# Kernel optimization log

Measured on AMD Instinct MI355X. Metric: run time of the kernel, lower is better.

Reference implementation:

```python
import jax, jax.numpy as jnp
import numpy as np

EPS = 1e-06
NUM_HEADS = 16


def _rms_norm(x, g, eps=EPS):
    # normalize over the last (full model) dim, as WanRMSNorm(dim)
    var = jnp.mean(jnp.square(x), axis=-1, keepdims=True)
    return x * jax.lax.rsqrt(var + eps) * g


def _apply_rope(q, k, freqs):
    # q, k: [b, s, n, d]; freqs: [s, d//2] angles. Interleaved (complex) pairs
    b, s, n, d = q.shape
    cos = jnp.cos(freqs)[None, :, None, :]  # [1, s, 1, d//2]
    sin = jnp.sin(freqs)[None, :, None, :]

    def rot(t):
        tr = t.reshape(b, s, n, d // 2, 2)
        t0, t1 = tr[..., 0], tr[..., 1]
        o0 = t0 * cos - t1 * sin
        o1 = t0 * sin + t1 * cos
        return jnp.stack([o0, o1], axis=-1).reshape(b, s, n, d)

    return rot(q), rot(k)


def setup_inputs() -> dict:
    key = jax.random.key(0)
    ks = jax.random.split(key, 8)
    b, s, dim = 2, 2048, 2048
    hd = dim // NUM_HEADS
    x = jax.random.normal(ks[0], (b, s, dim), dtype=jnp.float32)
    seq_lens = jax.random.randint(ks[1], (b,), s // 2, s + 1, dtype=jnp.int32)
    grid_sizes = jax.random.randint(ks[2], (b, 3), 1, 16).astype(jnp.int64)
    freqs = jax.random.uniform(ks[3], (s, hd // 2), dtype=jnp.float32) * 6.283
    sc = 1.0 / np.sqrt(dim)
    Wq = jax.random.normal(ks[4], (dim, dim), dtype=jnp.float32) * sc
    Wk = jax.random.normal(ks[5], (dim, dim), dtype=jnp.float32) * sc
    Wv = jax.random.normal(ks[6], (dim, dim), dtype=jnp.float32) * sc
    Wo = jax.random.normal(ks[7], (dim, dim), dtype=jnp.float32) * sc
    bo = jnp.zeros((dim,), dtype=jnp.float32)
    gq = jnp.ones((dim,), dtype=jnp.float32)
    gk = jnp.ones((dim,), dtype=jnp.float32)
    return {"x": x, "seq_lens": seq_lens, "grid_sizes": grid_sizes, "freqs": freqs,
            "Wq": Wq, "Wk": Wk, "Wv": Wv, "Wo": Wo, "bo": bo, "gq": gq, "gk": gk}


def reference(x, seq_lens, grid_sizes, freqs, Wq, Wk, Wv, Wo, bo, gq, gk):
    b, s, dim = x.shape
    n = NUM_HEADS
    d = dim // n
    scale = d ** (-0.5)

    # QKV projections (Linear: x @ W.T), with RMSNorm over full dim on q/k
    q = _rms_norm(x @ Wq.T, gq).reshape(b, s, n, d)
    k = _rms_norm(x @ Wk.T, gk).reshape(b, s, n, d)
    v = (x @ Wv.T).reshape(b, s, n, d)

    q, k = _apply_rope(q, k, freqs)

    # varlen attention: keys beyond seq_lens[b] are masked out
    scores = jnp.einsum("bqnd,bknd->bnqk", q, k) * scale
    key_valid = jnp.arange(s)[None, None, None, :] < seq_lens[:, None, None, None]
    scores = jnp.where(key_valid, scores, jnp.float32(-1e9))
    probs = jax.nn.softmax(scores, axis=-1)
    attn = jnp.einsum("bnqk,bknd->bqnd", probs, v).reshape(b, s, dim)

    return attn @ Wo.T + bo
```

## Files before the change

### kernel.cpp

```cpp
#include <hip/hip_runtime.h>
#include <hip/hip_bf16.h>
#include <math.h>

#define BATCH 2
#define SEQ   2048
#define DIM   2048
#define NH    16
#define HD    128
#define NROWS (BATCH * SEQ)
#define EPS_RMS 1e-6f

typedef unsigned short ushort_t;
typedef unsigned int   uint_t;
typedef __bf16    bf16x8 __attribute__((ext_vector_type(8)));
typedef _Float16  f16x8  __attribute__((ext_vector_type(8)));
typedef float     f32x4  __attribute__((ext_vector_type(4)));

__device__ inline ushort_t f2bf(float f) {
    uint_t u = __builtin_bit_cast(uint_t, f);
    uint_t r = u + 0x7FFFu + ((u >> 16) & 1u);
    return (ushort_t)(r >> 16);
}
__device__ inline ushort_t f2h(float f) {
    return __builtin_bit_cast(ushort_t, (_Float16)f);
}

__global__ __launch_bounds__(256) void cvt_all_kernel(
    const float* __restrict__ x,  const float* __restrict__ wq,
    const float* __restrict__ wk, const float* __restrict__ wv,
    const float* __restrict__ wo,
    ushort_t* __restrict__ xh,  ushort_t* __restrict__ wqh,
    ushort_t* __restrict__ wkh, ushort_t* __restrict__ wvh,
    ushort_t* __restrict__ woh)
{
    const int blk = blockIdx.x;
    const float* src; ushort_t* dst; size_t base;
    if (blk < 4096) { src = x; dst = xh; base = (size_t)blk * 2048; }
    else {
        const int r = blk - 4096;
        const int wsel = r >> 11;
        base = (size_t)(r & 2047) * 2048;
        if      (wsel == 0) { src = wq; dst = wqh; }
        else if (wsel == 1) { src = wk; dst = wkh; }
        else if (wsel == 2) { src = wv; dst = wvh; }
        else                { src = wo; dst = woh; }
    }
    const size_t i = base + ((size_t)threadIdx.x << 3);
    float v[8];
    *(float4*)&v[0] = *(const float4*)&src[i];
    *(float4*)&v[4] = *(const float4*)&src[i + 4];
    uint_t pk[4];
#pragma unroll
    for (int j = 0; j < 4; ++j)
        pk[j] = (uint_t)f2h(v[2 * j]) | ((uint_t)f2h(v[2 * j + 1]) << 16);
    *(uint4*)&dst[i] = make_uint4(pk[0], pk[1], pk[2], pk[3]);
}

template<int MODE>
__global__ __launch_bounds__(256, 3) void gemm_f16_kernel(
    const ushort_t* __restrict__ Ah, const ushort_t* __restrict__ Bh,
    const float* __restrict__ bias,
    float* __restrict__ C, ushort_t* __restrict__ Ct,
    const int M, const int N, const int K)
{
    __shared__ __align__(16) ushort_t sA[4096], sB[4096];
    const int tid  = threadIdx.x;
    const int w    = tid >> 6;
    const int lane = tid & 63;

    const int bid   = blockIdx.x;
    const int chunk = gridDim.x >> 3;
    const int nid   = (bid & 7) * chunk + (bid >> 3);
    const int mb    = M >> 7;
    const int n_blk = nid / mb;
    const int m_blk = nid - n_blk * mb;
    const int m0 = m_blk * 128;
    const int n0 = n_blk * 128;

    const int scol = (lane & 3) << 3;
    const int wr = w >> 1, wc = w & 1;
    const int fr = lane & 15, quad = lane >> 4;

    f32x4 acc[4][4];
#pragma unroll
    for (int mi = 0; mi < 4; ++mi)
#pragma unroll
        for (int ni = 0; ni < 4; ++ni)
            acc[mi][ni] = (f32x4){0.f, 0.f, 0.f, 0.f};

    for (int k0 = 0; k0 < K; k0 += 32) {
        __syncthreads();
#pragma unroll
        for (int it = 0; it < 2; ++it) {
            const int row  = (w << 5) + (it << 4) + (lane >> 2);
            const int loff = (w << 10) + (it << 9);
            const size_t ga = (size_t)(m0 + row) * K + k0 + scol;
            const size_t gb = (size_t)(n0 + row) * K + k0 + scol;
            __builtin_amdgcn_global_load_lds(
                (const __attribute__((address_space(1))) uint_t*)(const void*)(Ah + ga),
                (__attribute__((address_space(3))) uint_t*)(void*)&sA[loff], 16, 0, 0);
            __builtin_amdgcn_global_load_lds(
                (const __attribute__((address_space(1))) uint_t*)(const void*)(Bh + gb),
                (__attribute__((address_space(3))) uint_t*)(void*)&sB[loff], 16, 0, 0);
        }
        __syncthreads();

        f16x8 bfr[4];
#pragma unroll
        for (int ni = 0; ni < 4; ++ni) {
            const int row = (wc << 6) + (ni << 4) + fr;
            bfr[ni] = *(const f16x8*)&sB[(row << 5) + (quad << 3)];
        }
#pragma unroll
        for (int mi = 0; mi < 4; ++mi) {
            const int row = (wr << 6) + (mi << 4) + fr;
            const f16x8 ah = *(const f16x8*)&sA[(row << 5) + (quad << 3)];
#pragma unroll
            for (int ni = 0; ni < 4; ++ni)
                acc[mi][ni] = __builtin_amdgcn_mfma_f32_16x16x32_f16(ah, bfr[ni], acc[mi][ni], 0, 0, 0);
        }
    }

#pragma unroll
    for (int mi = 0; mi < 4; ++mi)
#pragma unroll
        for (int ni = 0; ni < 4; ++ni) {
            const int col = n0 + (wc << 6) + (ni << 4) + fr;
            if (MODE == 0) {
                const float bv = bias ? bias[col] : 0.f;
#pragma unroll
                for (int r = 0; r < 4; ++r) {
                    const int rowg = m0 + (wr << 6) + (mi << 4) + (quad << 2) + r;
                    C[(size_t)rowg * N + col] = acc[mi][ni][r] + bv;
                }
            } else {
                const int rowg = m0 + (wr << 6) + (mi << 4) + (quad << 2);
                const int bb = rowg >> 11, tok = rowg & (SEQ - 1);
                const int hh = col >> 7, d = col & (HD - 1);
                uint2 pk;
                pk.x = (uint_t)f2bf(acc[mi][ni][0]) | ((uint_t)f2bf(acc[mi][ni][1]) << 16);
                pk.y = (uint_t)f2bf(acc[mi][ni][2]) | ((uint_t)f2bf(acc[mi][ni][3]) << 16);
                *(uint2*)&Ct[((size_t)(bb * NH + hh) * HD + d) * SEQ + tok] = pk;
            }
        }
}

__global__ __launch_bounds__(512, 2) void qkv_gemm_kernel(
    const ushort_t* __restrict__ Ah, const ushort_t* __restrict__ Bq,
    const ushort_t* __restrict__ Bk, const ushort_t* __restrict__ Bv,
    float* __restrict__ Qb, float* __restrict__ Kb, ushort_t* __restrict__ Vt)
{
    __shared__ __align__(16) ushort_t sA[16384];
    __shared__ __align__(16) ushort_t sB[32768];
    const int tid  = threadIdx.x;
    const int w    = tid >> 6;
    const int lane = tid & 63;
    const int fr   = lane & 15;
    const int quad = lane >> 4;
    const int wr   = w >> 2;
    const int wc   = w & 3;

    const int bid   = blockIdx.x;
    const int nid   = (bid & 7) * 96 + (bid >> 3);
    const int n_blk = nid >> 5;
    const int m_blk = nid & 31;
    const int wsel  = n_blk >> 3;
    const int m0    = m_blk << 7;
    const int n0    = (n_blk & 7) << 8;
    const ushort_t* __restrict__ Bh = (wsel == 0) ? Bq : (wsel == 1) ? Bk : Bv;

    const int rt  = tid >> 3;
    const int csw = ((tid & 7) ^ (rt & 7)) << 3;
    const size_t abg = (size_t)(m0 + rt) * DIM + csw;
    const size_t bbg = (size_t)(n0 + rt) * DIM + csw;
    const int lw  = w << 9;
    const int axor = (fr & 7) << 4;

#define QG(dst, src) __builtin_amdgcn_global_load_lds( \
        (const __attribute__((address_space(1))) uint_t*)(const void*)(src), \
        (__attribute__((address_space(3))) uint_t*)(void*)(dst), 16, 0, 0)
#define QSA(buf, kt, p) QG(sA + ((buf) << 13) + ((p) << 12) + lw, \
                           Ah + abg + ((size_t)(p) << 17) + ((size_t)(kt) << 6))
#define QSB(buf, kt, p) QG(sB + ((buf) << 14) + ((p) << 12) + lw, \
                           Bh + bbg + ((size_t)(p) << 17) + ((size_t)(kt) << 6))

    f32x4 acc[4][4];
#pragma unroll
    for (int mi = 0; mi < 4; ++mi)
#pragma unroll
        for (int ni = 0; ni < 4; ++ni)
            acc[mi][ni] = (f32x4){0.f, 0.f, 0.f, 0.f};

#pragma unroll
    for (int p = 0; p < 2; ++p) QSA(0, 0, p);
#pragma unroll
    for (int p = 0; p < 4; ++p) QSB(0, 0, p);
#pragma unroll
    for (int p = 0; p < 2; ++p) QSA(1, 1, p);
#pragma unroll
    for (int p = 0; p < 4; ++p) QSB(1, 1, p);
    asm volatile("s_waitcnt vmcnt(6)" ::: "memory");
    __builtin_amdgcn_sched_barrier(0);
    __builtin_amdgcn_s_barrier();
    __builtin_amdgcn_sched_barrier(0);

#define QPHASE(MB)                                                              \
        {                                                                       \
            f16x8 af[2][2];                                                     \
            _Pragma("unroll")                                                   \
            for (int m2 = 0; m2 < 2; ++m2)                                      \
                _Pragma("unroll")                                               \
                for (int ks = 0; ks < 2; ++ks)                                  \
                    af[m2][ks] = *(const f16x8*)(sAc +                          \
                        (((wr << 6) + (((MB) + m2) << 4) + fr) << 7) +          \
                        (((ks << 6) + (quad << 4)) ^ axor));                    \
            __builtin_amdgcn_s_setprio(1);                                      \
            _Pragma("unroll")                                                   \
            for (int ks = 0; ks < 2; ++ks)                                      \
                _Pragma("unroll")                                               \
                for (int m2 = 0; m2 < 2; ++m2)                                  \
                    _Pragma("unroll")                                           \
                    for (int ni = 0; ni < 4; ++ni)                              \
                        acc[(MB) + m2][ni] = __builtin_amdgcn_mfma_f32_16x16x32_f16( \
                            af[m2][ks], bfr[ni][ks], acc[(MB) + m2][ni], 0, 0, 0); \
            __builtin_amdgcn_s_setprio(0);                                      \
        }                                                                       \
        __builtin_amdgcn_sched_barrier(0);                                      \
        __builtin_amdgcn_s_barrier();                                           \
        __builtin_amdgcn_sched_barrier(0);

    for (int kt = 0; kt < 32; ++kt) {
        const int cur = kt & 1;
        const char* sAc = (const char*)sA + (cur << 14);
        const char* sBc = (const char*)sB + (cur << 15);
        const bool pf = (kt < 30);

        f16x8 bfr[4][2];
#pragma unroll
        for (int ni = 0; ni < 4; ++ni) {
            const int brow = (wc << 6) + (ni << 4) + fr;
#pragma unroll
            for (int ks = 0; ks < 2; ++ks)
                bfr[ni][ks] = *(const f16x8*)(sBc + brow * 128 +
                    (((ks << 6) + (quad << 4)) ^ axor));
        }
        QPHASE(0)
        if (pf) { QSB(cur, kt + 2, 0); QSB(cur, kt + 2, 1);
                  QSB(cur, kt + 2, 2); QSB(cur, kt + 2, 3); }
        QPHASE(2)
        if (pf) {
            QSA(cur, kt + 2, 0); QSA(cur, kt + 2, 1);
            asm volatile("s_waitcnt vmcnt(6)" ::: "memory");
        } else {
            asm volatile("s_waitcnt vmcnt(0)" ::: "memory");
        }
        __builtin_amdgcn_sched_barrier(0);
        __builtin_amdgcn_s_barrier();
        __builtin_amdgcn_sched_barrier(0);
    }
#undef QPHASE
#undef QSA
#undef QSB
#undef QG

    if (wsel < 2) {
        float* __restrict__ C = (wsel == 0) ? Qb : Kb;
#pragma unroll
        for (int mi = 0; mi < 4; ++mi)
#pragma unroll
            for (int ni = 0; ni < 4; ++ni) {
                const int col = n0 + (wc << 6) + (ni << 4) + fr;
#pragma unroll
                for (int r = 0; r < 4; ++r) {
                    const int rowg = m0 + (wr << 6) + (mi << 4) + (quad << 2) + r;
                    C[(size_t)rowg * DIM + col] = acc[mi][ni][r];
                }
            }
    } else {
#pragma unroll
        for (int mi = 0; mi < 4; ++mi)
#pragma unroll
            for (int ni = 0; ni < 4; ++ni) {
                const int col = n0 + (wc << 6) + (ni << 4) + fr;
                const int rowg = m0 + (wr << 6) + (mi << 4) + (quad << 2);
                const int bbi = rowg >> 11, tok = rowg & (SEQ - 1);
                const int hh = col >> 7, d = col & (HD - 1);
                uint2 pk;
                pk.x = (uint_t)f2bf(acc[mi][ni][0]) | ((uint_t)f2bf(acc[mi][ni][1]) << 16);
                pk.y = (uint_t)f2bf(acc[mi][ni][2]) | ((uint_t)f2bf(acc[mi][ni][3]) << 16);
                *(uint2*)&Vt[((size_t)(bbi * NH + hh) * HD + d) * SEQ + tok] = pk;
            }
    }
}

#define BM 64
#define BN 64
#define BK 16

__global__ __launch_bounds__(256) void gemm_nt_kernel(
    const float* __restrict__ A, const float* __restrict__ W,
    const float* __restrict__ bias, float* __restrict__ C,
    const int M, const int N, const int K)
{
    __shared__ float As[BK][BM + 4];
    __shared__ float Bs[BK][BN + 4];
    const int tid = threadIdx.x;
    const int tx = tid & 15;
    const int ty = tid >> 4;
    const int m0 = blockIdx.y * BM;
    const int n0 = blockIdx.x * BN;
    const int ldr = tid >> 2;
    const int ldc = (tid & 3) << 2;

    float acc[4][4] = {};

    for (int k0 = 0; k0 < K; k0 += BK) {
        __syncthreads();
        const float4 av = *(const float4*)&A[(size_t)(m0 + ldr) * K + (k0 + ldc)];
        const float4 wv = *(const float4*)&W[(size_t)(n0 + ldr) * K + (k0 + ldc)];
        As[ldc + 0][ldr] = av.x; As[ldc + 1][ldr] = av.y;
        As[ldc + 2][ldr] = av.z; As[ldc + 3][ldr] = av.w;
        Bs[ldc + 0][ldr] = wv.x; Bs[ldc + 1][ldr] = wv.y;
        Bs[ldc + 2][ldr] = wv.z; Bs[ldc + 3][ldr] = wv.w;
        __syncthreads();
#pragma unroll
        for (int k = 0; k < BK; ++k) {
            const float4 a4 = *(const float4*)&As[k][ty << 2];
            const float4 b4 = *(const float4*)&Bs[k][tx << 2];
            const float aa[4] = {a4.x, a4.y, a4.z, a4.w};
            const float bb[4] = {b4.x, b4.y, b4.z, b4.w};
#pragma unroll
            for (int i = 0; i < 4; ++i)
#pragma unroll
                for (int j = 0; j < 4; ++j)
                    acc[i][j] = fmaf(aa[i], bb[j], acc[i][j]);
        }
    }

#pragma unroll
    for (int i = 0; i < 4; ++i) {
        const int row = m0 + (ty << 2) + i;
        const int col = n0 + (tx << 2);
        float4 ov;
        ov.x = acc[i][0]; ov.y = acc[i][1]; ov.z = acc[i][2]; ov.w = acc[i][3];
        if (bias != nullptr) {
            ov.x += bias[col + 0]; ov.y += bias[col + 1];
            ov.z += bias[col + 2]; ov.w += bias[col + 3];
        }
        *(float4*)&C[(size_t)row * N + col] = ov;
    }
}

__global__ __launch_bounds__(256) void rmsnorm_rope_qk_kernel(
    const float* __restrict__ Qb, const float* __restrict__ gq,
    ushort_t* __restrict__ qbh,
    const float* __restrict__ Kb, const float* __restrict__ gk,
    ushort_t* __restrict__ kbh,
    const float* __restrict__ freqs)
{
    const int r = blockIdx.x;
    const int s = r & (SEQ - 1);
    const int tid = threadIdx.x;
    const int base = tid << 3;
    const bool isQ = (blockIdx.y == 0);
    const float* T = isQ ? Qb : Kb;
    const float* g = isQ ? gq : gk;
    ushort_t* out  = isQ ? qbh : kbh;
    const float posc = isQ ? 0.088388347648318447f : 1.0f;

    float v[8];
    *(float4*)&v[0] = *(const float4*)&T[(size_t)r * DIM + base];
    *(float4*)&v[4] = *(const float4*)&T[(size_t)r * DIM + base + 4];

    float ss = 0.f;
#pragma unroll
    for (int i = 0; i < 8; ++i) ss += v[i] * v[i];
#pragma unroll
    for (int off = 32; off > 0; off >>= 1) ss += __shfl_down(ss, off);

    __shared__ float wsum[4];
    __shared__ float inv_sh;
    if ((tid & 63) == 0) wsum[tid >> 6] = ss;
    __syncthreads();
    if (tid == 0)
        inv_sh = rsqrtf((wsum[0] + wsum[1] + wsum[2] + wsum[3]) * (1.0f / DIM) + EPS_RMS);
    __syncthreads();
    const float inv = inv_sh * posc;

    float gg[8];
    *(float4*)&gg[0] = *(const float4*)&g[base];
    *(float4*)&gg[4] = *(const float4*)&g[base + 4];
#pragma unroll
    for (int i = 0; i < 8; ++i) v[i] *= inv * gg[i];

    const int p0 = (base & (HD - 1)) >> 1;
#pragma unroll
    for (int pp = 0; pp < 4; ++pp) {
        float sn, cs;
        __sincosf(freqs[(size_t)s * (HD / 2) + p0 + pp], &sn, &cs);
        const float t0 = v[2 * pp], t1 = v[2 * pp + 1];
        v[2 * pp]     = t0 * cs - t1 * sn;
        v[2 * pp + 1] = t0 * sn + t1 * cs;
    }

    uint_t pk[4];
#pragma unroll
    for (int j = 0; j < 4; ++j)
        pk[j] = (uint_t)f2bf(v[2 * j]) | ((uint_t)f2bf(v[2 * j + 1]) << 16);
    *(uint4*)&out[(size_t)r * DIM + base] = make_uint4(pk[0], pk[1], pk[2], pk[3]);
}

__global__ __launch_bounds__(256) void rmsnorm_rope_kernel(
    float* __restrict__ T, const float* __restrict__ g,
    const float* __restrict__ freqs)
{
    const int r = blockIdx.x;
    const int s = r & (SEQ - 1);
    const int tid = threadIdx.x;
    const int base = tid << 3;

    float v[8];
    *(float4*)&v[0] = *(const float4*)&T[(size_t)r * DIM + base];
    *(float4*)&v[4] = *(const float4*)&T[(size_t)r * DIM + base + 4];

    float ss = 0.f;
#pragma unroll
    for (int i = 0; i < 8; ++i) ss += v[i] * v[i];
#pragma unroll
    for (int off = 32; off > 0; off >>= 1) ss += __shfl_down(ss, off);

    __shared__ float wsum[4];
    __shared__ float inv_sh;
    if ((tid & 63) == 0) wsum[tid >> 6] = ss;
    __syncthreads();
    if (tid == 0)
        inv_sh = rsqrtf((wsum[0] + wsum[1] + wsum[2] + wsum[3]) * (1.0f / DIM) + EPS_RMS);
    __syncthreads();
    const float inv = inv_sh;

    float gg[8];
    *(float4*)&gg[0] = *(const float4*)&g[base];
    *(float4*)&gg[4] = *(const float4*)&g[base + 4];
#pragma unroll
    for (int i = 0; i < 8; ++i) v[i] *= inv * gg[i];

    const int p0 = (base & (HD - 1)) >> 1;
#pragma unroll
    for (int pp = 0; pp < 4; ++pp) {
        float sn, cs;
        __sincosf(freqs[(size_t)s * (HD / 2) + p0 + pp], &sn, &cs);
        const float t0 = v[2 * pp], t1 = v[2 * pp + 1];
        v[2 * pp]     = t0 * cs - t1 * sn;
        v[2 * pp + 1] = t0 * sn + t1 * cs;
    }

    *(float4*)&T[(size_t)r * DIM + base]     = *(float4*)&v[0];
    *(float4*)&T[(size_t)r * DIM + base + 4] = *(float4*)&v[4];
}

#define AQ 128
#define AK 64
#define KSTR 136
#define VSTR 72
#define RESCALE_THR 8.0f

__global__ __launch_bounds__(256, 3) void attn_mfma_kernel(
    const ushort_t* __restrict__ QH, const ushort_t* __restrict__ KH,
    const ushort_t* __restrict__ VtG, const int* __restrict__ seq_lens,
    ushort_t* __restrict__ Oh)
{
    __shared__ __align__(16) ushort_t sK[AK * KSTR];
    __shared__ __align__(16) ushort_t sVt[HD * VSTR];
    __shared__ __align__(16) ushort_t sP[AQ * VSTR];

    const int tid  = threadIdx.x;
    const int w    = tid >> 6;
    const int lane = tid & 63;
    const int fr   = lane & 15;
    const int quad = lane >> 4;

    const int bid = blockIdx.x;
    const int sw  = (bid & 7) * 64 + (bid >> 3);
    const int q0  = (sw & 15) * AQ;
    const int hb  = sw >> 4;
    const int h   = hb & 15;
    const int b   = hb >> 4;
    const int len = seq_lens[b];

    bf16x8 qfrag[2][4];
#pragma unroll
    for (int qt = 0; qt < 2; ++qt)
#pragma unroll
        for (int h4 = 0; h4 < 4; ++h4) {
            const size_t qrow = (size_t)(b * SEQ + q0 + (w << 5) + (qt << 4) + fr);
            qfrag[qt][h4] = *(const bf16x8*)&QH[qrow * DIM + h * HD + (h4 << 5) + (quad << 3)];
        }

    f32x4 Oacc[2][8];
#pragma unroll
    for (int qt = 0; qt < 2; ++qt)
#pragma unroll
        for (int dt = 0; dt < 8; ++dt)
            Oacc[qt][dt] = (f32x4){0.f, 0.f, 0.f, 0.f};
    float mrow[2] = {-1.0e30f, -1.0e30f};
    float lrow[2] = {0.f, 0.f};

    const int kr  = tid >> 4;
    const int kc8 = (tid & 15) << 3;
    const int vd  = tid >> 3;
    const int vc8 = (tid & 7) << 3;
    const size_t kbase = (size_t)(b * SEQ) * DIM + h * HD + kc8;
    const size_t vbase = ((size_t)(b * NH + h) * HD) * SEQ + vc8;

    const int ntiles = (len + AK - 1) / AK;
    for (int t = 0; t < ntiles; ++t) {
        const int k0 = t * AK;
        const bool masked = (k0 + AK > len);
        __syncthreads();
        {
            uint4 kv[4], vv[4];
#pragma unroll
            for (int j = 0; j < 4; ++j)
                kv[j] = *(const uint4*)&KH[kbase + (size_t)(k0 + kr + (j << 4)) * DIM];
#pragma unroll
            for (int j = 0; j < 4; ++j)
                vv[j] = *(const uint4*)&VtG[vbase + (size_t)(vd + (j << 5)) * SEQ + k0];
#pragma unroll
            for (int j = 0; j < 4; ++j)
                *(uint4*)&sK[(kr + (j << 4)) * KSTR + kc8] = kv[j];
#pragma unroll
            for (int j = 0; j < 4; ++j)
                *(uint4*)&sVt[(vd + (j << 5)) * VSTR + vc8] = vv[j];
        }
        __syncthreads();

        f32x4 S[4][2];
        __builtin_amdgcn_s_setprio(1);
#pragma unroll
        for (int kt = 0; kt < 4; ++kt) {
            bf16x8 kf[4];
#pragma unroll
            for (int h4 = 0; h4 < 4; ++h4)
                kf[h4] = *(const bf16x8*)&sK[((kt << 4) + fr) * KSTR + (h4 << 5) + (quad << 3)];
#pragma unroll
            for (int qt = 0; qt < 2; ++qt) {
                f32x4 a = (f32x4){0.f, 0.f, 0.f, 0.f};
#pragma unroll
                for (int h4 = 0; h4 < 4; ++h4)
                    a = __builtin_amdgcn_mfma_f32_16x16x32_bf16(kf[h4], qfrag[qt][h4], a, 0, 0, 0);
                S[kt][qt] = a;
            }
        }
        __builtin_amdgcn_s_setprio(0);

#pragma unroll
        for (int qt = 0; qt < 2; ++qt) {
            float tm = -1.0e30f;
            if (masked) {
#pragma unroll
                for (int kt = 0; kt < 4; ++kt)
#pragma unroll
                    for (int r = 0; r < 4; ++r) {
                        const int key = k0 + (kt << 4) + (quad << 2) + r;
                        float s = (key < len) ? S[kt][qt][r] : -1.0e30f;
                        S[kt][qt][r] = s;
                        tm = fmaxf(tm, s);
                    }
            } else {
#pragma unroll
                for (int kt = 0; kt < 4; ++kt)
#pragma unroll
                    for (int r = 0; r < 4; ++r)
                        tm = fmaxf(tm, S[kt][qt][r]);
            }
            tm = fmaxf(tm, __shfl_xor(tm, 16));
            tm = fmaxf(tm, __shfl_xor(tm, 32));

            float mnew;
            if (__all(tm - mrow[qt] <= RESCALE_THR)) {
                mnew = mrow[qt];
            } else {
                mnew = fmaxf(mrow[qt], tm);
                const float alpha = __expf(mrow[qt] - mnew);
                mrow[qt] = mnew;
                lrow[qt] *= alpha;
#pragma unroll
                for (int r = 0; r < 4; ++r) {
                    const float ar = __shfl(alpha, (quad << 2) + r);
#pragma unroll
                    for (int dt = 0; dt < 8; ++dt)
                        Oacc[qt][dt][r] *= ar;
                }
            }

            float rsum = 0.f;
#pragma unroll
            for (int kt = 0; kt < 4; ++kt) {
                float p[4];
#pragma unroll
                for (int r = 0; r < 4; ++r) {
                    p[r] = __expf(S[kt][qt][r] - mnew);
                    rsum += p[r];
                }
                uint2 pk;
                pk.x = (uint_t)f2bf(p[0]) | ((uint_t)f2bf(p[1]) << 16);
                pk.y = (uint_t)f2bf(p[2]) | ((uint_t)f2bf(p[3]) << 16);
                *(uint2*)&sP[((w << 5) + (qt << 4) + fr) * VSTR + (kt << 4) + (quad << 2)] = pk;
            }
            rsum += __shfl_xor(rsum, 16);
            rsum += __shfl_xor(rsum, 32);
            lrow[qt] += rsum;
        }

        __builtin_amdgcn_s_setprio(1);
#pragma unroll
        for (int ks = 0; ks < 2; ++ks) {
            bf16x8 pf[2];
#pragma unroll
            for (int qt = 0; qt < 2; ++qt)
                pf[qt] = *(const bf16x8*)&sP[((w << 5) + (qt << 4) + fr) * VSTR + (ks << 5) + (quad << 3)];
#pragma unroll
            for (int dt = 0; dt < 8; ++dt) {
                const bf16x8 vf = *(const bf16x8*)&sVt[((dt << 4) + fr) * VSTR + (ks << 5) + (quad << 3)];
#pragma unroll
                for (int qt = 0; qt < 2; ++qt)
                    Oacc[qt][dt] = __builtin_amdgcn_mfma_f32_16x16x32_bf16(pf[qt], vf, Oacc[qt][dt], 0, 0, 0);
            }
        }
        __builtin_amdgcn_s_setprio(0);
    }

#pragma unroll
    for (int qt = 0; qt < 2; ++qt) {
        float linv[4];
#pragma unroll
        for (int r = 0; r < 4; ++r)
            linv[r] = 1.0f / __shfl(lrow[qt], (quad << 2) + r);
#pragma unroll
        for (int dt = 0; dt < 8; ++dt)
#pragma unroll
            for (int r = 0; r < 4; ++r) {
                const int qrow = q0 + (w << 5) + (qt << 4) + (quad << 2) + r;
                Oh[(size_t)(b * SEQ + qrow) * DIM + h * HD + (dt << 4) + fr] =
                    f2h(Oacc[qt][dt][r] * linv[r]);
            }
    }
}

#define BQ  64
#define BKT 64

__global__ __launch_bounds__(256) void attn_kernel(
    const float* __restrict__ Q, const float* __restrict__ K,
    const float* __restrict__ V, const int* __restrict__ seq_lens,
    float* __restrict__ O)
{
    const int qt = blockIdx.x;
    const int h  = blockIdx.y;
    const int b  = blockIdx.z;
    const int len = seq_lens[b];
    const int q0 = qt * BQ;
    const float scale = 0.088388347648318447f;

    __shared__ float Qst[HD][BQ + 4];
    __shared__ float Kst[HD][BKT + 4];
    __shared__ float Vs[BKT][HD + 4];
    __shared__ float Sc[BQ][BKT + 1];
    __shared__ float mrow[BQ], lrow[BQ], alpha_s[BQ];

    const int tid = threadIdx.x;
    const int si0 = (tid >> 4) << 2;
    const int sj0 = (tid & 15) << 2;
    const int pi0 = (tid >> 4) << 2;
    const int pc0 = (tid & 15) << 3;

    for (int i = tid; i < BQ * HD / 4; i += 256) {
        const int e = i << 2;
        const int row = e >> 7;
        const int c0 = e & (HD - 1);
        const float4 qv = *(const float4*)&Q[(size_t)(b * SEQ + q0 + row) * DIM + h * HD + c0];
        Qst[c0 + 0][row] = qv.x; Qst[c0 + 1][row] = qv.y;
        Qst[c0 + 2][row] = qv.z; Qst[c0 + 3][row] = qv.w;
    }
    if (tid < BQ) { mrow[tid] = -3.0e38f; lrow[tid] = 0.f; }

    float o[4][8] = {};
    __syncthreads();

    const int ntiles = (len + BKT - 1) / BKT;
    for (int t = 0; t < ntiles; ++t) {
        const int k0 = t * BKT;
        __syncthreads();
        for (int i = tid; i < BKT * HD / 4; i += 256) {
            const int e = i << 2;
            const int row = e >> 7;
            const int c0 = e & (HD - 1);
            const int kg = k0 + row;
            float4 kv = make_float4(0.f, 0.f, 0.f, 0.f);
            float4 vv = make_float4(0.f, 0.f, 0.f, 0.f);
            if (kg < len) {
                kv = *(const float4*)&K[(size_t)(b * SEQ + kg) * DIM + h * HD + c0];
                vv = *(const float4*)&V[(size_t)(b * SEQ + kg) * DIM + h * HD + c0];
            }
            Kst[c0 + 0][row] = kv.x; Kst[c0 + 1][row] = kv.y;
            Kst[c0 + 2][row] = kv.z; Kst[c0 + 3][row] = kv.w;
            *(float4*)&Vs[row][c0] = vv;
        }
        __syncthreads();

        float acc[4][4] = {};
#pragma unroll 8
        for (int kk = 0; kk < HD; ++kk) {
            const float4 q4 = *(const float4*)&Qst[kk][si0];
            const float4 k4 = *(const float4*)&Kst[kk][sj0];
            const float qa[4] = {q4.x, q4.y, q4.z, q4.w};
            const float ka[4] = {k4.x, k4.y, k4.z, k4.w};
#pragma unroll
            for (int i = 0; i < 4; ++i)
#pragma unroll
                for (int j = 0; j < 4; ++j)
                    acc[i][j] = fmaf(qa[i], ka[j], acc[i][j]);
        }
#pragma unroll
        for (int i = 0; i < 4; ++i)
#pragma unroll
            for (int j = 0; j < 4; ++j) {
                const int jg = k0 + sj0 + j;
                Sc[si0 + i][sj0 + j] = (jg < len) ? acc[i][j] * scale : -1.0e9f;
            }
        __syncthreads();

        if (tid < BQ) {
            const int i = tid;
            const float m_old = mrow[i];
            float mx = m_old;
            for (int j = 0; j < BKT; ++j) mx = fmaxf(mx, Sc[i][j]);
            const float al = __expf(m_old - mx);
            float sum = 0.f;
            for (int j = 0; j < BKT; ++j) {
                const float p = __expf(Sc[i][j] - mx);
                Sc[i][j] = p;
                sum += p;
            }
            mrow[i] = mx;
            lrow[i] = lrow[i] * al + sum;
            alpha_s[i] = al;
        }
        __syncthreads();

#pragma unroll
        for (int i = 0; i < 4; ++i) {
            const float al = alpha_s[pi0 + i];
#pragma unroll
            for (int c = 0; c < 8; ++c) o[i][c] *= al;
        }
        for (int j = 0; j < BKT; ++j) {
            float p[4];
#pragma unroll
            for (int i = 0; i < 4; ++i) p[i] = Sc[pi0 + i][j];
            const float4 v0 = *(const float4*)&Vs[j][pc0];
            const float4 v1 = *(const float4*)&Vs[j][pc0 + 4];
            const float va[8] = {v0.x, v0.y, v0.z, v0.w, v1.x, v1.y, v1.z, v1.w};
#pragma unroll
            for (int i = 0; i < 4; ++i)
#pragma unroll
                for (int c = 0; c < 8; ++c)
                    o[i][c] = fmaf(p[i], va[c], o[i][c]);
        }
    }

#pragma unroll
    for (int i = 0; i < 4; ++i) {
        const float invl = 1.0f / lrow[pi0 + i];
        float4 w0, w1;
        w0.x = o[i][0] * invl; w0.y = o[i][1] * invl;
        w0.z = o[i][2] * invl; w0.w = o[i][3] * invl;
        w1.x = o[i][4] * invl; w1.y = o[i][5] * invl;
        w1.z = o[i][6] * invl; w1.w = o[i][7] * invl;
        float* op = &O[(size_t)(b * SEQ + q0 + pi0 + i) * DIM + h * HD + pc0];
        *(float4*)&op[0] = w0;
        *(float4*)&op[4] = w1;
    }
}

extern "C" void kernel_launch(void* const* d_in, const int* in_sizes, int n_in,
                              void* d_out, int out_size, void* d_ws, size_t ws_size,
                              hipStream_t stream)
{
    const float* x        = (const float*)d_in[0];
    const int*   seq_lens = (const int*)d_in[1];
    const float* freqs    = (const float*)d_in[3];
    const float* Wq       = (const float*)d_in[4];
    const float* Wk       = (const float*)d_in[5];
    const float* Wv       = (const float*)d_in[6];
    const float* Wo       = (const float*)d_in[7];
    const float* bo       = (const float*)d_in[8];
    const float* gq       = (const float*)d_in[9];
    const float* gk       = (const float*)d_in[10];
    float* out = (float*)d_out;

    const size_t mat = (size_t)NROWS * DIM;
    const size_t wsz = (size_t)DIM * DIM;

    float*    Qb   = (float*)d_ws;
    float*    Kb   = Qb + mat;
    ushort_t* xh   = (ushort_t*)(Kb + mat);
    ushort_t* wqh  = xh + mat;
    ushort_t* wkh  = wqh + wsz;
    ushort_t* wvh  = wkh + wsz;
    ushort_t* woh  = wvh + wsz;
    ushort_t* qbh  = woh + wsz;
    ushort_t* kbh  = qbh + mat;
    ushort_t* vtg  = kbh + mat;
    ushort_t* abh  = vtg + mat;

    const size_t need = 2 * mat * sizeof(float)
                      + (mat + 4 * wsz + 4 * mat) * sizeof(ushort_t);

    if (ws_size >= need) {
        cvt_all_kernel<<<12288, 256, 0, stream>>>(
            x, Wq, Wk, Wv, Wo, xh, wqh, wkh, wvh, woh);

        qkv_gemm_kernel<<<768, 512, 0, stream>>>(xh, wqh, wkh, wvh, Qb, Kb, vtg);

        rmsnorm_rope_qk_kernel<<<dim3(NROWS, 2), 256, 0, stream>>>(
            Qb, gq, qbh, Kb, gk, kbh, freqs);

        attn_mfma_kernel<<<512, 256, 0, stream>>>(qbh, kbh, vtg, seq_lens, abh);

        gemm_f16_kernel<0><<<512, 256, 0, stream>>>(abh, woh, bo, out, nullptr, NROWS, DIM, DIM);
    } else {
        float* Vb = Kb + mat;
        float* Ab = Vb + mat;
        const dim3 gemm_grid(DIM / BN, NROWS / BM);
        gemm_nt_kernel<<<gemm_grid, 256, 0, stream>>>(x, Wq, nullptr, Qb, NROWS, DIM, DIM);
        gemm_nt_kernel<<<gemm_grid, 256, 0, stream>>>(x, Wk, nullptr, Kb, NROWS, DIM, DIM);
        gemm_nt_kernel<<<gemm_grid, 256, 0, stream>>>(x, Wv, nullptr, Vb, NROWS, DIM, DIM);
        rmsnorm_rope_kernel<<<NROWS, 256, 0, stream>>>(Qb, gq, freqs);
        rmsnorm_rope_kernel<<<NROWS, 256, 0, stream>>>(Kb, gk, freqs);
        attn_kernel<<<dim3(SEQ / BQ, NH, BATCH), 256, 0, stream>>>(Qb, Kb, Vb, seq_lens, Ab);
        gemm_nt_kernel<<<gemm_grid, 256, 0, stream>>>(Ab, Wo, bo, out, NROWS, DIM, DIM);
    }
}
```

Measured before the change: 452.4 us.

## Triple-buffer QKV GEMM LDS tiles and issue prefetch at iteration start

The QKV projection GEMM moves from a two-slot LDS ring, where next-tile loads were interleaved between MFMA phases, to a three-slot ring. All loads for tile kt+2 are issued at the top of each iteration into a free slot. The intra-iteration barriers and sched_barriers go away, leaving one wait and one barrier per k-step, which is meant to reduce synchronisation stalls and widen load/compute overlap. LDS use grows from 96KB to 144KB per block, which can cut the two-blocks-per-CU occupancy implied by the launch bounds. The waitcnt of 6 on the last prefetched iteration now also covers fewer outstanding loads, so correctness depends on the count still matching.

```diff
diff --git a/kernel.cpp b/kernel.cpp
--- a/kernel.cpp
+++ b/kernel.cpp
@@ -150,8 +150,8 @@
     const ushort_t* __restrict__ Bk, const ushort_t* __restrict__ Bv,
     float* __restrict__ Qb, float* __restrict__ Kb, ushort_t* __restrict__ Vt)
 {
-    __shared__ __align__(16) ushort_t sA[16384];
-    __shared__ __align__(16) ushort_t sB[32768];
+    __shared__ __align__(16) ushort_t sA[24576];
+    __shared__ __align__(16) ushort_t sB[49152];
     const int tid  = threadIdx.x;
     const int w    = tid >> 6;
     const int lane = tid & 63;
@@ -179,10 +179,12 @@
 #define QG(dst, src) __builtin_amdgcn_global_load_lds( \
         (const __attribute__((address_space(1))) uint_t*)(const void*)(src), \
         (__attribute__((address_space(3))) uint_t*)(void*)(dst), 16, 0, 0)
-#define QSA(buf, kt, p) QG(sA + ((buf) << 13) + ((p) << 12) + lw, \
+#define QSA(buf, kt, p) QG(sA + (buf) * 8192 + ((p) << 12) + lw, \
                            Ah + abg + ((size_t)(p) << 17) + ((size_t)(kt) << 6))
-#define QSB(buf, kt, p) QG(sB + ((buf) << 14) + ((p) << 12) + lw, \
+#define QSB(buf, kt, p) QG(sB + (buf) * 16384 + ((p) << 12) + lw, \
                            Bh + bbg + ((size_t)(p) << 17) + ((size_t)(kt) << 6))
+#define STAGE(buf, kt) { QSB(buf, kt, 0); QSB(buf, kt, 1); QSB(buf, kt, 2); \
+                         QSB(buf, kt, 3); QSA(buf, kt, 0); QSA(buf, kt, 1); }
 
     f32x4 acc[4][4];
 #pragma unroll
@@ -191,49 +193,21 @@
         for (int ni = 0; ni < 4; ++ni)
             acc[mi][ni] = (f32x4){0.f, 0.f, 0.f, 0.f};
 
-#pragma unroll
-    for (int p = 0; p < 2; ++p) QSA(0, 0, p);
-#pragma unroll
-    for (int p = 0; p < 4; ++p) QSB(0, 0, p);
-#pragma unroll
-    for (int p = 0; p < 2; ++p) QSA(1, 1, p);
-#pragma unroll
-    for (int p = 0; p < 4; ++p) QSB(1, 1, p);
+    STAGE(0, 0)
+    STAGE(1, 1)
     asm volatile("s_waitcnt vmcnt(6)" ::: "memory");
-    __builtin_amdgcn_sched_barrier(0);
     __builtin_amdgcn_s_barrier();
-    __builtin_amdgcn_sched_barrier(0);
-
-#define QPHASE(MB)                                                              \
-        {                                                                       \
-            f16x8 af[2][2];                                                     \
-            _Pragma("unroll")                                                   \
-            for (int m2 = 0; m2 < 2; ++m2)                                      \
-                _Pragma("unroll")                                               \
-                for (int ks = 0; ks < 2; ++ks)                                  \
-                    af[m2][ks] = *(const f16x8*)(sAc +                          \
-                        (((wr << 6) + (((MB) + m2) << 4) + fr) << 7) +          \
-                        (((ks << 6) + (quad << 4)) ^ axor));                    \
-            __builtin_amdgcn_s_setprio(1);                                      \
-            _Pragma("unroll")                                                   \
-            for (int ks = 0; ks < 2; ++ks)                                      \
-                _Pragma("unroll")                                               \
-                for (int m2 = 0; m2 < 2; ++m2)                                  \
-                    _Pragma("unroll")                                           \
-                    for (int ni = 0; ni < 4; ++ni)                              \
-                        acc[(MB) + m2][ni] = __builtin_amdgcn_mfma_f32_16x16x32_f16( \
-                            af[m2][ks], bfr[ni][ks], acc[(MB) + m2][ni], 0, 0, 0); \
-            __builtin_amdgcn_s_setprio(0);                                      \
-        }                                                                       \
-        __builtin_amdgcn_sched_barrier(0);                                      \
-        __builtin_amdgcn_s_barrier();                                           \
-        __builtin_amdgcn_sched_barrier(0);
-
+
+    int cur = 0;
     for (int kt = 0; kt < 32; ++kt) {
-        const int cur = kt & 1;
-        const char* sAc = (const char*)sA + (cur << 14);
-        const char* sBc = (const char*)sB + (cur << 15);
         const bool pf = (kt < 30);
+        if (pf) {
+            const int nb = (cur + 2 >= 3) ? cur - 1 : cur + 2;
+            STAGE(nb, kt + 2)
+        }
+
+        const char* sAc = (const char*)sA + cur * 16384;
+        const char* sBc = (const char*)sB + cur * 32768;
 
         f16x8 bfr[4][2];
 #pragma unroll
@@ -244,21 +218,35 @@
                 bfr[ni][ks] = *(const f16x8*)(sBc + brow * 128 +
                     (((ks << 6) + (quad << 4)) ^ axor));
         }
-        QPHASE(0)
-        if (pf) { QSB(cur, kt + 2, 0); QSB(cur, kt + 2, 1);
-                  QSB(cur, kt + 2, 2); QSB(cur, kt + 2, 3); }
-        QPHASE(2)
-        if (pf) {
-            QSA(cur, kt + 2, 0); QSA(cur, kt + 2, 1);
-            asm volatile("s_waitcnt vmcnt(6)" ::: "memory");
-        } else {
-            asm volatile("s_waitcnt vmcnt(0)" ::: "memory");
-        }
-        __builtin_amdgcn_sched_barrier(0);
+#pragma unroll
+        for (int MB = 0; MB < 4; MB += 2) {
+            f16x8 af[2][2];
+#pragma unroll
+            for (int m2 = 0; m2 < 2; ++m2)
+#pragma unroll
+                for (int ks = 0; ks < 2; ++ks)
+                    af[m2][ks] = *(const f16x8*)(sAc +
+                        (((wr << 6) + ((MB + m2) << 4) + fr) << 7) +
+                        (((ks << 6) + (quad << 4)) ^ axor));
+            __builtin_amdgcn_s_setprio(1);
+#pragma unroll
+            for (int ks = 0; ks < 2; ++ks)
+#pragma unroll
+                for (int m2 = 0; m2 < 2; ++m2)
+#pragma unroll
+                    for (int ni = 0; ni < 4; ++ni)
+                        acc[MB + m2][ni] = __builtin_amdgcn_mfma_f32_16x16x32_f16(
+                            af[m2][ks], bfr[ni][ks], acc[MB + m2][ni], 0, 0, 0);
+            __builtin_amdgcn_s_setprio(0);
+        }
+
+        if (pf) asm volatile("s_waitcnt vmcnt(6)" ::: "memory");
+        else    asm volatile("s_waitcnt vmcnt(0)" ::: "memory");
         __builtin_amdgcn_s_barrier();
-        __builtin_amdgcn_sched_barrier(0);
-    }
-#undef QPHASE
+
+        cur = (cur + 1 >= 3) ? 0 : cur + 1;
+    }
+#undef STAGE
 #undef QSA
 #undef QSB
 #undef QG
```

New measurement: 459.1 us. No clear change (+1.5%).

## Replace output projection GEMM with pipelined 128x256 kernel; store Q/K as fp16

Applied to the files above, without the earlier changes.

Swaps the simple single-buffered 128x128 output projection GEMM for a 512-thread kernel with double-buffered LDS, XOR-swizzled layout and async global-to-LDS prefetch, mirroring the QKV GEMM design. Separately, the QKV GEMM now writes Q and K as fp16 instead of fp32, which halves the intermediate traffic into the RMSNorm/RoPE kernel. The fp16 storage of unnormalized Q/K adds rounding and could overflow for large activations. The new GEMM launches only 256 blocks, which may underfill the GPU.

```diff
diff --git a/kernel.cpp b/kernel.cpp
--- a/kernel.cpp
+++ b/kernel.cpp
@@ -23,6 +23,9 @@
 }
 __device__ inline ushort_t f2h(float f) {
     return __builtin_bit_cast(ushort_t, (_Float16)f);
+}
+__device__ inline float h2f(ushort_t h) {
+    return (float)__builtin_bit_cast(_Float16, h);
 }
 
 __global__ __launch_bounds__(256) void cvt_all_kernel(
@@ -56,99 +59,10 @@
     *(uint4*)&dst[i] = make_uint4(pk[0], pk[1], pk[2], pk[3]);
 }
 
-template<int MODE>
-__global__ __launch_bounds__(256, 3) void gemm_f16_kernel(
-    const ushort_t* __restrict__ Ah, const ushort_t* __restrict__ Bh,
-    const float* __restrict__ bias,
-    float* __restrict__ C, ushort_t* __restrict__ Ct,
-    const int M, const int N, const int K)
-{
-    __shared__ __align__(16) ushort_t sA[4096], sB[4096];
-    const int tid  = threadIdx.x;
-    const int w    = tid >> 6;
-    const int lane = tid & 63;
-
-    const int bid   = blockIdx.x;
-    const int chunk = gridDim.x >> 3;
-    const int nid   = (bid & 7) * chunk + (bid >> 3);
-    const int mb    = M >> 7;
-    const int n_blk = nid / mb;
-    const int m_blk = nid - n_blk * mb;
-    const int m0 = m_blk * 128;
-    const int n0 = n_blk * 128;
-
-    const int scol = (lane & 3) << 3;
-    const int wr = w >> 1, wc = w & 1;
-    const int fr = lane & 15, quad = lane >> 4;
-
-    f32x4 acc[4][4];
-#pragma unroll
-    for (int mi = 0; mi < 4; ++mi)
-#pragma unroll
-        for (int ni = 0; ni < 4; ++ni)
-            acc[mi][ni] = (f32x4){0.f, 0.f, 0.f, 0.f};
-
-    for (int k0 = 0; k0 < K; k0 += 32) {
-        __syncthreads();
-#pragma unroll
-        for (int it = 0; it < 2; ++it) {
-            const int row  = (w << 5) + (it << 4) + (lane >> 2);
-            const int loff = (w << 10) + (it << 9);
-            const size_t ga = (size_t)(m0 + row) * K + k0 + scol;
-            const size_t gb = (size_t)(n0 + row) * K + k0 + scol;
-            __builtin_amdgcn_global_load_lds(
-                (const __attribute__((address_space(1))) uint_t*)(const void*)(Ah + ga),
-                (__attribute__((address_space(3))) uint_t*)(void*)&sA[loff], 16, 0, 0);
-            __builtin_amdgcn_global_load_lds(
-                (const __attribute__((address_space(1))) uint_t*)(const void*)(Bh + gb),
-                (__attribute__((address_space(3))) uint_t*)(void*)&sB[loff], 16, 0, 0);
-        }
-        __syncthreads();
-
-        f16x8 bfr[4];
-#pragma unroll
-        for (int ni = 0; ni < 4; ++ni) {
-            const int row = (wc << 6) + (ni << 4) + fr;
-            bfr[ni] = *(const f16x8*)&sB[(row << 5) + (quad << 3)];
-        }
-#pragma unroll
-        for (int mi = 0; mi < 4; ++mi) {
-            const int row = (wr << 6) + (mi << 4) + fr;
-            const f16x8 ah = *(const f16x8*)&sA[(row << 5) + (quad << 3)];
-#pragma unroll
-            for (int ni = 0; ni < 4; ++ni)
-                acc[mi][ni] = __builtin_amdgcn_mfma_f32_16x16x32_f16(ah, bfr[ni], acc[mi][ni], 0, 0, 0);
-        }
-    }
-
-#pragma unroll
-    for (int mi = 0; mi < 4; ++mi)
-#pragma unroll
-        for (int ni = 0; ni < 4; ++ni) {
-            const int col = n0 + (wc << 6) + (ni << 4) + fr;
-            if (MODE == 0) {
-                const float bv = bias ? bias[col] : 0.f;
-#pragma unroll
-                for (int r = 0; r < 4; ++r) {
-                    const int rowg = m0 + (wr << 6) + (mi << 4) + (quad << 2) + r;
-                    C[(size_t)rowg * N + col] = acc[mi][ni][r] + bv;
-                }
-            } else {
-                const int rowg = m0 + (wr << 6) + (mi << 4) + (quad << 2);
-                const int bb = rowg >> 11, tok = rowg & (SEQ - 1);
-                const int hh = col >> 7, d = col & (HD - 1);
-                uint2 pk;
-                pk.x = (uint_t)f2bf(acc[mi][ni][0]) | ((uint_t)f2bf(acc[mi][ni][1]) << 16);
-                pk.y = (uint_t)f2bf(acc[mi][ni][2]) | ((uint_t)f2bf(acc[mi][ni][3]) << 16);
-                *(uint2*)&Ct[((size_t)(bb * NH + hh) * HD + d) * SEQ + tok] = pk;
-            }
-        }
-}
-
 __global__ __launch_bounds__(512, 2) void qkv_gemm_kernel(
     const ushort_t* __restrict__ Ah, const ushort_t* __restrict__ Bq,
     const ushort_t* __restrict__ Bk, const ushort_t* __restrict__ Bv,
-    float* __restrict__ Qb, float* __restrict__ Kb, ushort_t* __restrict__ Vt)
+    ushort_t* __restrict__ Qh, ushort_t* __restrict__ Kh, ushort_t* __restrict__ Vt)
 {
     __shared__ __align__(16) ushort_t sA[16384];
     __shared__ __align__(16) ushort_t sB[32768];
@@ -264,7 +178,7 @@
 #undef QG
 
     if (wsel < 2) {
-        float* __restrict__ C = (wsel == 0) ? Qb : Kb;
+        ushort_t* __restrict__ C = (wsel == 0) ? Qh : Kh;
 #pragma unroll
         for (int mi = 0; mi < 4; ++mi)
 #pragma unroll
@@ -273,7 +187,7 @@
 #pragma unroll
                 for (int r = 0; r < 4; ++r) {
                     const int rowg = m0 + (wr << 6) + (mi << 4) + (quad << 2) + r;
-                    C[(size_t)rowg * DIM + col] = acc[mi][ni][r];
+                    C[(size_t)rowg * DIM + col] = f2h(acc[mi][ni][r]);
                 }
             }
     } else {
@@ -291,6 +205,135 @@
                 *(uint2*)&Vt[((size_t)(bbi * NH + hh) * HD + d) * SEQ + tok] = pk;
             }
     }
+}
+
+__global__ __launch_bounds__(512, 2) void wo_gemm_kernel(
+    const ushort_t* __restrict__ Ah, const ushort_t* __restrict__ Bh,
+    const float* __restrict__ bias, float* __restrict__ C)
+{
+    __shared__ __align__(16) ushort_t sA[16384];
+    __shared__ __align__(16) ushort_t sB[32768];
+    const int tid  = threadIdx.x;
+    const int w    = tid >> 6;
+    const int lane = tid & 63;
+    const int fr   = lane & 15;
+    const int quad = lane >> 4;
+    const int wr   = w >> 2;
+    const int wc   = w & 3;
+
+    const int bid   = blockIdx.x;
+    const int nid   = (bid & 7) * 32 + (bid >> 3);
+    const int n_blk = nid >> 5;
+    const int m_blk = nid & 31;
+    const int m0    = m_blk << 7;
+    const int n0    = n_blk << 8;
+
+    const int rt  = tid >> 3;
+    const int csw = ((tid & 7) ^ (rt & 7)) << 3;
+    const size_t abg = (size_t)(m0 + rt) * DIM + csw;
+    const size_t bbg = (size_t)(n0 + rt) * DIM + csw;
+    const int lw  = w << 9;
+    const int axor = (fr & 7) << 4;
+
+#define QG(dst, src) __builtin_amdgcn_global_load_lds( \
+        (const __attribute__((address_space(1))) uint_t*)(const void*)(src), \
+        (__attribute__((address_space(3))) uint_t*)(void*)(dst), 16, 0, 0)
+#define QSA(buf, kt, p) QG(sA + ((buf) << 13) + ((p) << 12) + lw, \
+                           Ah + abg + ((size_t)(p) << 17) + ((size_t)(kt) << 6))
+#define QSB(buf, kt, p) QG(sB + ((buf) << 14) + ((p) << 12) + lw, \
+                           Bh + bbg + ((size_t)(p) << 17) + ((size_t)(kt) << 6))
+
+    f32x4 acc[4][4];
+#pragma unroll
+    for (int mi = 0; mi < 4; ++mi)
+#pragma unroll
+        for (int ni = 0; ni < 4; ++ni)
+            acc[mi][ni] = (f32x4){0.f, 0.f, 0.f, 0.f};
+
+#pragma unroll
+    for (int p = 0; p < 2; ++p) QSA(0, 0, p);
+#pragma unroll
+    for (int p = 0; p < 4; ++p) QSB(0, 0, p);
+#pragma unroll
+    for (int p = 0; p < 2; ++p) QSA(1, 1, p);
+#pragma unroll
+    for (int p = 0; p < 4; ++p) QSB(1, 1, p);
+    asm volatile("s_waitcnt vmcnt(6)" ::: "memory");
+    __builtin_amdgcn_sched_barrier(0);
+    __builtin_amdgcn_s_barrier();
+    __builtin_amdgcn_sched_barrier(0);
+
+#define QPHASE(MB)                                                              \
+        {                                                                       \
+            f16x8 af[2][2];                                                     \
+            _Pragma("unroll")                                                   \
+            for (int m2 = 0; m2 < 2; ++m2)                                      \
+                _Pragma("unroll")                                               \
+                for (int ks = 0; ks < 2; ++ks)                                  \
+                    af[m2][ks] = *(const f16x8*)(sAc +                          \
+                        (((wr << 6) + (((MB) + m2) << 4) + fr) << 7) +          \
+                        (((ks << 6) + (quad << 4)) ^ axor));                    \
+            __builtin_amdgcn_s_setprio(1);                                      \
+            _Pragma("unroll")                                                   \
+            for (int ks = 0; ks < 2; ++ks)                                      \
+                _Pragma("unroll")                                               \
+                for (int m2 = 0; m2 < 2; ++m2)                                  \
+                    _Pragma("unroll")                                           \
+                    for (int ni = 0; ni < 4; ++ni)                              \
+                        acc[(MB) + m2][ni] = __builtin_amdgcn_mfma_f32_16x16x32_f16( \
+                            af[m2][ks], bfr[ni][ks], acc[(MB) + m2][ni], 0, 0, 0); \
+            __builtin_amdgcn_s_setprio(0);                                      \
+        }                                                                       \
+        __builtin_amdgcn_sched_barrier(0);                                      \
+        __builtin_amdgcn_s_barrier();                                           \
+        __builtin_amdgcn_sched_barrier(0);
+
+    for (int kt = 0; kt < 32; ++kt) {
+        const int cur = kt & 1;
+        const char* sAc = (const char*)sA + (cur << 14);
+        const char* sBc = (const char*)sB + (cur << 15);
+        const bool pf = (kt < 30);
+
+        f16x8 bfr[4][2];
+#pragma unroll
+        for (int ni = 0; ni < 4; ++ni) {
+            const int brow = (wc << 6) + (ni << 4) + fr;
+#pragma unroll
+            for (int ks = 0; ks < 2; ++ks)
+                bfr[ni][ks] = *(const f16x8*)(sBc + brow * 128 +
+                    (((ks << 6) + (quad << 4)) ^ axor));
+        }
+        QPHASE(0)
+        if (pf) { QSB(cur, kt + 2, 0); QSB(cur, kt + 2, 1);
+                  QSB(cur, kt + 2, 2); QSB(cur, kt + 2, 3); }
+        QPHASE(2)
+        if (pf) {
+            QSA(cur, kt + 2, 0); QSA(cur, kt + 2, 1);
+            asm volatile("s_waitcnt vmcnt(6)" ::: "memory");
+        } else {
+            asm volatile("s_waitcnt vmcnt(0)" ::: "memory");
+        }
+        __builtin_amdgcn_sched_barrier(0);
+        __builtin_amdgcn_s_barrier();
+        __builtin_amdgcn_sched_barrier(0);
+    }
+#undef QPHASE
+#undef QSA
+#undef QSB
+#undef QG
+
+#pragma unroll
+    for (int mi = 0; mi < 4; ++mi)
+#pragma unroll
+        for (int ni = 0; ni < 4; ++ni) {
+            const int col = n0 + (wc << 6) + (ni << 4) + fr;
+            const float bv = bias[col];
+#pragma unroll
+            for (int r = 0; r < 4; ++r) {
+                const int rowg = m0 + (wr << 6) + (mi << 4) + (quad << 2) + r;
+                C[(size_t)rowg * DIM + col] = acc[mi][ni][r] + bv;
+            }
+        }
 }
 
 #define BM 64
@@ -352,9 +395,9 @@
 }
 
 __global__ __launch_bounds__(256) void rmsnorm_rope_qk_kernel(
-    const float* __restrict__ Qb, const float* __restrict__ gq,
+    const ushort_t* __restrict__ Qh, const float* __restrict__ gq,
     ushort_t* __restrict__ qbh,
-    const float* __restrict__ Kb, const float* __restrict__ gk,
+    const ushort_t* __restrict__ Kh, const float* __restrict__ gk,
     ushort_t* __restrict__ kbh,
     const float* __restrict__ freqs)
 {
@@ -363,14 +406,16 @@
     const int tid = threadIdx.x;
     const int base = tid << 3;
     const bool isQ = (blockIdx.y == 0);
-    const float* T = isQ ? Qb : Kb;
+    const ushort_t* T = isQ ? Qh : Kh;
     const float* g = isQ ? gq : gk;
     ushort_t* out  = isQ ? qbh : kbh;
     const float posc = isQ ? 0.088388347648318447f : 1.0f;
 
+    const uint4 raw = *(const uint4*)&T[(size_t)r * DIM + base];
+    const ushort_t* rp = (const ushort_t*)&raw;
     float v[8];
-    *(float4*)&v[0] = *(const float4*)&T[(size_t)r * DIM + base];
-    *(float4*)&v[4] = *(const float4*)&T[(size_t)r * DIM + base + 4];
+#pragma unroll
+    for (int i = 0; i < 8; ++i) v[i] = h2f(rp[i]);
 
     float ss = 0.f;
 #pragma unroll
@@ -802,9 +847,9 @@
     const size_t mat = (size_t)NROWS * DIM;
     const size_t wsz = (size_t)DIM * DIM;
 
-    float*    Qb   = (float*)d_ws;
-    float*    Kb   = Qb + mat;
-    ushort_t* xh   = (ushort_t*)(Kb + mat);
+    ushort_t* qh16 = (ushort_t*)d_ws;
+    ushort_t* kh16 = qh16 + mat;
+    ushort_t* xh   = kh16 + 3 * mat;
     ushort_t* wqh  = xh + mat;
     ushort_t* wkh  = wqh + wsz;
     ushort_t* wvh  = wkh + wsz;
@@ -821,15 +866,17 @@
         cvt_all_kernel<<<12288, 256, 0, stream>>>(
             x, Wq, Wk, Wv, Wo, xh, wqh, wkh, wvh, woh);
 
-        qkv_gemm_kernel<<<768, 512, 0, stream>>>(xh, wqh, wkh, wvh, Qb, Kb, vtg);
+        qkv_gemm_kernel<<<768, 512, 0, stream>>>(xh, wqh, wkh, wvh, qh16, kh16, vtg);
 
         rmsnorm_rope_qk_kernel<<<dim3(NROWS, 2), 256, 0, stream>>>(
-            Qb, gq, qbh, Kb, gk, kbh, freqs);
+            qh16, gq, qbh, kh16, gk, kbh, freqs);
 
         attn_mfma_kernel<<<512, 256, 0, stream>>>(qbh, kbh, vtg, seq_lens, abh);
 
-        gemm_f16_kernel<0><<<512, 256, 0, stream>>>(abh, woh, bo, out, nullptr, NROWS, DIM, DIM);
+        wo_gemm_kernel<<<256, 512, 0, stream>>>(abh, woh, bo, out);
     } else {
+        float* Qb = (float*)d_ws;
+        float* Kb = Qb + mat;
         float* Vb = Kb + mat;
         float* Ab = Vb + mat;
         const dim3 gemm_grid(DIM / BN, NROWS / BM);
```

After: 448.7 us, median of 3. About the same (-0.8%).
